# Performance work log

Measured on AMD Instinct MI355X. Metric: run time of the kernel, lower is better.

## Reference

```python
import jax, jax.numpy as jnp
import numpy as np

D_MODEL = 1024
NUM_HEADS = 16
DEPTH = D_MODEL // NUM_HEADS


def setup_inputs() -> dict:
    key = jax.random.key(0)
    ks = jax.random.split(key, 9)
    B, S = 2, 2048
    s = 1.0 / np.sqrt(D_MODEL)
    inp = {
        "inputs": jax.random.normal(ks[0], (B, S, D_MODEL), dtype=jnp.float32),
        "wq": jax.random.normal(ks[1], (D_MODEL, D_MODEL), dtype=jnp.float32) * s,
        "bq": jnp.zeros((D_MODEL,), dtype=jnp.float32),
        "wk": jax.random.normal(ks[2], (D_MODEL, D_MODEL), dtype=jnp.float32) * s,
        "bk": jnp.zeros((D_MODEL,), dtype=jnp.float32),
        "wv": jax.random.normal(ks[3], (D_MODEL, D_MODEL), dtype=jnp.float32) * s,
        "bv": jnp.zeros((D_MODEL,), dtype=jnp.float32),
        "wo": jax.random.normal(ks[4], (D_MODEL, D_MODEL), dtype=jnp.float32) * s,
        "bo": jnp.zeros((D_MODEL,), dtype=jnp.float32),
    }
    return inp


def _split_heads(x, B):
    # [B, S, D] -> [B, H, S, depth]
    S = x.shape[1]
    return x.reshape(B, S, NUM_HEADS, DEPTH).transpose(0, 2, 1, 3)


def reference(inputs, wq, bq, wk, bk, wv, bv, wo, bo):
    B, S, _ = inputs.shape
    q = _split_heads(inputs @ wq + bq, B)  # [B,H,S,d]
    k = _split_heads(inputs @ wk + bk, B)
    v = _split_heads(inputs @ wv + bv, B)
    scale = 1.0 / jnp.sqrt(jnp.asarray(DEPTH, dtype=inputs.dtype))
    logits = jnp.einsum("bhqd,bhkd->bhqk", q, k) * scale  # [B,H,S,S]
    attn = jax.nn.softmax(logits, axis=-1)
    out = jnp.einsum("bhqk,bhkd->bhqd", attn, v)  # [B,H,S,d]
    out = out.transpose(0, 2, 1, 3).reshape(B, S, D_MODEL)
    return out @ wo + bo
```

## Files before the change

kernel.cpp:

```cpp
#include <hip/hip_runtime.h>
#include <math.h>

#define SEQ     2048
#define DM      1024
#define NH      16
#define DEPTH   64
#define MTOT    4096

typedef __attribute__((ext_vector_type(8))) __bf16 bf16x8;
typedef __attribute__((ext_vector_type(4))) float  f32x4;
typedef __attribute__((ext_vector_type(4))) short  short4v;

static __device__ inline short f2bf(float f) {
    union { float f; unsigned u; } v; v.f = f;
    unsigned r = v.u + 0x7FFFu + ((v.u >> 16) & 1u);
    return (short)(r >> 16);
}
static __device__ inline unsigned bfbits(float f) {
    union { float f; unsigned u; } v; v.f = f;
    return (v.u + 0x7FFFu + ((v.u >> 16) & 1u)) >> 16;
}
static __device__ inline unsigned bfbits_fast(float f) {
    union { float f; unsigned u; } v; v.f = f;
    return (v.u + 0x8000u) >> 16;
}

#define GLOBAL_AS(p) ((const __attribute__((address_space(1))) void*)(p))
#define LDS_AS(p)    ((__attribute__((address_space(3))) void*)(p))

#define K2  0.18033688011112043f
#define C2 -17.31234049066756f
#define EXP2(x) __builtin_amdgcn_exp2f(x)

#define DMA_SRC_C8(lane)  ((((lane) & 3) ^ (((lane) >> 3) & 3)) * 8)
#define FRAG_C8(lx,quad)  ((((quad) ^ (((lx) >> 1) & 3))) * 8)

__global__ __launch_bounds__(256)
void prep(const float* __restrict__ X,
          const float* __restrict__ w0, const float* __restrict__ w1,
          const float* __restrict__ w2, const float* __restrict__ w3,
          short* __restrict__ Xb,
          short* __restrict__ o0, short* __restrict__ o1,
          short* __restrict__ o2, short* __restrict__ o3) {
    const int t = threadIdx.x;
    const int z = blockIdx.z;
    if (z >= 4) {
        int r0 = (z - 4) * 1024 + blockIdx.x * 64;
        int c0 = blockIdx.y * 64;
        #pragma unroll
        for (int i = 0; i < 4; i++) {
            int row = r0 + i * 16 + (t >> 4);
            int c4  = c0 + (t & 15) * 4;
            float4 v = *(const float4*)&X[(size_t)row * DM + c4];
            short4v o; o.x = f2bf(v.x); o.y = f2bf(v.y); o.z = f2bf(v.z); o.w = f2bf(v.w);
            *(short4v*)&Xb[(size_t)row * DM + c4] = o;
        }
        return;
    }
    const float* W; short* O;
    switch (z) {
        case 0: W = w0; O = o0; break;
        case 1: W = w1; O = o1; break;
        case 2: W = w2; O = o2; break;
        default: W = w3; O = o3; break;
    }
    __shared__ float Tf[64][65];
    const int k0 = blockIdx.x * 64, n0 = blockIdx.y * 64;
    #pragma unroll
    for (int i = 0; i < 4; i++) {
        int row = i * 16 + (t >> 4);
        int c4  = (t & 15) * 4;
        float4 v = *(const float4*)&W[(size_t)(k0 + row) * DM + n0 + c4];
        Tf[row][c4 + 0] = v.x; Tf[row][c4 + 1] = v.y;
        Tf[row][c4 + 2] = v.z; Tf[row][c4 + 3] = v.w;
    }
    __syncthreads();
    #pragma unroll
    for (int i = 0; i < 4; i++) {
        int nrow = i * 16 + (t >> 4);
        int kc4  = (t & 15) * 4;
        short4v o;
        o.x = f2bf(Tf[kc4 + 0][nrow]); o.y = f2bf(Tf[kc4 + 1][nrow]);
        o.z = f2bf(Tf[kc4 + 2][nrow]); o.w = f2bf(Tf[kc4 + 3][nrow]);
        *(short4v*)&O[(size_t)(n0 + nrow) * DM + k0 + kc4] = o;
    }
}

__global__ __launch_bounds__(256)
void gemm_qkv(const short* __restrict__ Xb,
              const short* __restrict__ Wqt, const short* __restrict__ Wkt,
              const short* __restrict__ Wvt,
              const float* __restrict__ bq, const float* __restrict__ bk,
              const float* __restrict__ bv,
              short* __restrict__ Qw, short* __restrict__ Kw,
              short* __restrict__ Vtw) {
    const int z = blockIdx.z;
    const short* A; const short* B; const float* bias;
    if (z == 0)      { A = Xb;  B = Wqt; bias = bq; }
    else if (z == 1) { A = Xb;  B = Wkt; bias = bk; }
    else             { A = Wvt; B = Xb;  bias = bv; }
    const int bx = blockIdx.x;
    int m0, n0;
    if (z < 2) { n0 = (bx & 7) * 128; m0 = (bx >> 3) * 128; }
    else       { m0 = (bx & 7) * 128; n0 = (bx >> 3) * 128; }

    __shared__ short As[128 * 32];
    __shared__ short Bs[128 * 32];
    const int t = threadIdx.x, lane = t & 63, w = t >> 6;
    const int lx = lane & 15, quad = lane >> 4;
    const int wm = (w & 1) * 64, wn = (w >> 1) * 64;
    const int r = lane >> 2;
    const int cs8 = DMA_SRC_C8(lane);

    f32x4 acc[4][4];
    #pragma unroll
    for (int i = 0; i < 4; i++)
        #pragma unroll
        for (int j = 0; j < 4; j++)
            acc[i][j] = (f32x4){0.f, 0.f, 0.f, 0.f};

    const int fa = FRAG_C8(lx, quad);

    for (int k0 = 0; k0 < DM; k0 += 32) {
        #pragma unroll
        for (int j = 0; j < 2; j++) {
            int rb = (w * 2 + j) * 16;
            __builtin_amdgcn_global_load_lds(
                GLOBAL_AS(A + (size_t)(m0 + rb + r) * DM + k0 + cs8),
                LDS_AS(As + rb * 32), 16, 0, 0);
            __builtin_amdgcn_global_load_lds(
                GLOBAL_AS(B + (size_t)(n0 + rb + r) * DM + k0 + cs8),
                LDS_AS(Bs + rb * 32), 16, 0, 0);
        }
        __syncthreads();

        bf16x8 af[4], bfr[4];
        #pragma unroll
        for (int mt = 0; mt < 4; mt++)
            af[mt] = *(bf16x8*)&As[(wm + mt * 16 + lx) * 32 + fa];
        #pragma unroll
        for (int nt = 0; nt < 4; nt++)
            bfr[nt] = *(bf16x8*)&Bs[(wn + nt * 16 + lx) * 32 + fa];
        #pragma unroll
        for (int mt = 0; mt < 4; mt++)
            #pragma unroll
            for (int nt = 0; nt < 4; nt++)
                acc[mt][nt] = __builtin_amdgcn_mfma_f32_16x16x32_bf16(
                    af[mt], bfr[nt], acc[mt][nt], 0, 0, 0);
        __syncthreads();
    }

    if (z < 2) {
        short* Cp = (z == 0) ? Qw : Kw;
        #pragma unroll
        for (int mt = 0; mt < 4; mt++)
            #pragma unroll
            for (int nt = 0; nt < 4; nt++)
                #pragma unroll
                for (int reg = 0; reg < 4; reg++) {
                    int row = m0 + wm + mt * 16 + quad * 4 + reg;
                    int col = n0 + wn + nt * 16 + lx;
                    Cp[(size_t)row * DM + col] = f2bf(acc[mt][nt][reg] + bias[col]);
                }
    } else {
        int colbase = n0 + wn;
        int bsel    = colbase >> 11;
        int scolb   = colbase & 2047;
        int kb      = scolb & ~63;
        short* Vbh  = Vtw + (size_t)bsel * ((size_t)NH * DEPTH * SEQ);
        #pragma unroll
        for (int mt = 0; mt < 4; mt++) {
            #pragma unroll
            for (int reg = 0; reg < 4; reg++) {
                int row = m0 + wm + mt * 16 + quad * 4 + reg;
                float bb = bias[row];
                unsigned lo = bfbits(acc[mt][0][reg] + bb) | (bfbits(acc[mt][1][reg] + bb) << 16);
                unsigned hi = bfbits(acc[mt][2][reg] + bb) | (bfbits(acc[mt][3][reg] + bb) << 16);
                size_t base = (size_t)row * SEQ + kb + 2 * lx;
                *(unsigned*)&Vbh[base]      = lo;
                *(unsigned*)&Vbh[base + 32] = hi;
            }
        }
    }
}

__global__ __launch_bounds__(256)
void gemm_out(const short* __restrict__ A, const short* __restrict__ B,
              const float* __restrict__ bias, float* __restrict__ C) {
    __shared__ short As[128 * 32];
    __shared__ short Bs[64 * 32];
    const int t = threadIdx.x, lane = t & 63, w = t >> 6;
    const int lx = lane & 15, quad = lane >> 4;
    const int n0 = blockIdx.x * 64, m0 = blockIdx.y * 128;
    const int wm = (w & 1) * 64, wn = (w >> 1) * 32;
    const int r = lane >> 2;
    const int cs8 = DMA_SRC_C8(lane);
    const int fa  = FRAG_C8(lx, quad);

    f32x4 acc[4][2];
    #pragma unroll
    for (int i = 0; i < 4; i++)
        #pragma unroll
        for (int j = 0; j < 2; j++)
            acc[i][j] = (f32x4){0.f, 0.f, 0.f, 0.f};

    for (int k0 = 0; k0 < DM; k0 += 32) {
        #pragma unroll
        for (int j = 0; j < 2; j++) {
            int rb = w * 32 + j * 16;
            __builtin_amdgcn_global_load_lds(
                GLOBAL_AS(A + (size_t)(m0 + rb + r) * DM + k0 + cs8),
                LDS_AS(As + rb * 32), 16, 0, 0);
        }
        {
            int rb = w * 16;
            __builtin_amdgcn_global_load_lds(
                GLOBAL_AS(B + (size_t)(n0 + rb + r) * DM + k0 + cs8),
                LDS_AS(Bs + rb * 32), 16, 0, 0);
        }
        __syncthreads();

        bf16x8 af[4], bfr[2];
        #pragma unroll
        for (int mt = 0; mt < 4; mt++)
            af[mt] = *(bf16x8*)&As[(wm + mt * 16 + lx) * 32 + fa];
        #pragma unroll
        for (int nt = 0; nt < 2; nt++)
            bfr[nt] = *(bf16x8*)&Bs[(wn + nt * 16 + lx) * 32 + fa];
        #pragma unroll
        for (int mt = 0; mt < 4; mt++)
            #pragma unroll
            for (int nt = 0; nt < 2; nt++)
                acc[mt][nt] = __builtin_amdgcn_mfma_f32_16x16x32_bf16(
                    af[mt], bfr[nt], acc[mt][nt], 0, 0, 0);
        __syncthreads();
    }

    #pragma unroll
    for (int mt = 0; mt < 4; mt++)
        #pragma unroll
        for (int nt = 0; nt < 2; nt++)
            #pragma unroll
            for (int reg = 0; reg < 4; reg++) {
                int row = m0 + wm + mt * 16 + quad * 4 + reg;
                int col = n0 + wn + nt * 16 + lx;
                C[(size_t)row * DM + col] = acc[mt][nt][reg] + bias[col];
            }
}

__global__ __launch_bounds__(256)
void flash_mfma(const short* __restrict__ Q, const short* __restrict__ K,
                const short* __restrict__ Vt, short* __restrict__ O) {
    __shared__ short Ks[2][64 * 32];
    __shared__ short Vs[2][64 * 32];
    __shared__ short Ps[128 * 72];

    const int t = threadIdx.x, lane = t & 63, w = t >> 6;
    const int lx = lane & 15, quad = lane >> 4;
    const int h = blockIdx.y, bb = blockIdx.z;
    const int q0 = blockIdx.x * 128;
    const int r = lane >> 2;
    const int cs8 = DMA_SRC_C8(lane);
    const int fa  = FRAG_C8(lx, quad);

    bf16x8 qa[2][2];
    #pragma unroll
    for (int mt = 0; mt < 2; mt++)
        #pragma unroll
        for (int ks = 0; ks < 2; ks++)
            qa[mt][ks] = *(const bf16x8*)&Q[(size_t)(bb * SEQ + q0 + w * 32 + mt * 16 + lx) * DM
                                            + h * DEPTH + ks * 32 + quad * 8];

    f32x4 of[2][4];
    float l_acc[2][4];
    #pragma unroll
    for (int mt = 0; mt < 2; mt++) {
        #pragma unroll
        for (int dt = 0; dt < 4; dt++) of[mt][dt] = (f32x4){0.f, 0.f, 0.f, 0.f};
        #pragma unroll
        for (int reg = 0; reg < 4; reg++) l_acc[mt][reg] = 0.f;
    }

    const short* Kb = K  + (size_t)bb * SEQ * DM + h * DEPTH;
    const short* Vb = Vt + (size_t)(bb * NH + h) * DEPTH * SEQ;

    for (int kt = 0; kt < SEQ / 64; kt++) {
        __syncthreads();
        const int kbase = kt * 64;
        {
            const short* kg = Kb + (size_t)(kbase + w * 16 + r) * DM;
            __builtin_amdgcn_global_load_lds(GLOBAL_AS(kg + cs8),      LDS_AS(&Ks[0][w * 16 * 32]), 16, 0, 0);
            __builtin_amdgcn_global_load_lds(GLOBAL_AS(kg + 32 + cs8), LDS_AS(&Ks[1][w * 16 * 32]), 16, 0, 0);
            const short* vg = Vb + (size_t)(w * 16 + r) * SEQ + kbase;
            __builtin_amdgcn_global_load_lds(GLOBAL_AS(vg + cs8),      LDS_AS(&Vs[0][w * 16 * 32]), 16, 0, 0);
            __builtin_amdgcn_global_load_lds(GLOBAL_AS(vg + 32 + cs8), LDS_AS(&Vs[1][w * 16 * 32]), 16, 0, 0);
        }
        __syncthreads();

        f32x4 s[2][4];
        #pragma unroll
        for (int mt = 0; mt < 2; mt++)
            #pragma unroll
            for (int nt = 0; nt < 4; nt++)
                s[mt][nt] = (f32x4){0.f, 0.f, 0.f, 0.f};
        #pragma unroll
        for (int ks = 0; ks < 2; ks++) {
            bf16x8 kb[4];
            #pragma unroll
            for (int nt = 0; nt < 4; nt++)
                kb[nt] = *(bf16x8*)&Ks[ks][(nt * 16 + lx) * 32 + fa];
            #pragma unroll
            for (int mt = 0; mt < 2; mt++)
                #pragma unroll
                for (int nt = 0; nt < 4; nt++)
                    s[mt][nt] = __builtin_amdgcn_mfma_f32_16x16x32_bf16(
                        qa[mt][ks], kb[nt], s[mt][nt], 0, 0, 0);
        }

        #pragma unroll
        for (int mt = 0; mt < 2; mt++) {
            #pragma unroll
            for (int reg = 0; reg < 4; reg++) {
                float p0 = EXP2(fmaf(s[mt][0][reg], K2, C2));
                float p1 = EXP2(fmaf(s[mt][1][reg], K2, C2));
                float p2 = EXP2(fmaf(s[mt][2][reg], K2, C2));
                float p3 = EXP2(fmaf(s[mt][3][reg], K2, C2));
                l_acc[mt][reg] += (p0 + p1) + (p2 + p3);
                int rowoff = (w * 32 + mt * 16 + quad * 4 + reg) * 72;
                unsigned pk01 = bfbits_fast(p0) | (bfbits_fast(p1) << 16);
                unsigned pk23 = bfbits_fast(p2) | (bfbits_fast(p3) << 16);
                *(unsigned*)&Ps[rowoff + 2 * lx]      = pk01;
                *(unsigned*)&Ps[rowoff + 32 + 2 * lx] = pk23;
            }
        }

        #pragma unroll
        for (int ks = 0; ks < 2; ks++) {
            bf16x8 vb[4], pa[2];
            #pragma unroll
            for (int dt = 0; dt < 4; dt++)
                vb[dt] = *(bf16x8*)&Vs[ks][(dt * 16 + lx) * 32 + fa];
            #pragma unroll
            for (int mt = 0; mt < 2; mt++)
                pa[mt] = *(bf16x8*)&Ps[(w * 32 + mt * 16 + lx) * 72 + ks * 32 + quad * 8];
            #pragma unroll
            for (int mt = 0; mt < 2; mt++)
                #pragma unroll
                for (int dt = 0; dt < 4; dt++)
                    of[mt][dt] = __builtin_amdgcn_mfma_f32_16x16x32_bf16(
                        pa[mt], vb[dt], of[mt][dt], 0, 0, 0);
        }
    }

    #pragma unroll
    for (int mt = 0; mt < 2; mt++) {
        #pragma unroll
        for (int reg = 0; reg < 4; reg++) {
            float l = l_acc[mt][reg];
            l += __shfl_xor(l, 1);
            l += __shfl_xor(l, 2);
            l += __shfl_xor(l, 4);
            l += __shfl_xor(l, 8);
            float inv = 1.0f / l;
            size_t row = (size_t)bb * SEQ + q0 + w * 32 + mt * 16 + quad * 4 + reg;
            #pragma unroll
            for (int dt = 0; dt < 4; dt++)
                O[row * DM + h * DEPTH + dt * 16 + lx] = f2bf(of[mt][dt][reg] * inv);
        }
    }
}

extern "C" void kernel_launch(void* const* d_in, const int* in_sizes, int n_in,
                              void* d_out, int out_size, void* d_ws, size_t ws_size,
                              hipStream_t stream) {
    const float* X  = (const float*)d_in[0];
    const float* wq = (const float*)d_in[1];
    const float* bq = (const float*)d_in[2];
    const float* wk = (const float*)d_in[3];
    const float* bk = (const float*)d_in[4];
    const float* wv = (const float*)d_in[5];
    const float* bv = (const float*)d_in[6];
    const float* wo = (const float*)d_in[7];
    const float* bo = (const float*)d_in[8];
    float* out = (float*)d_out;

    short* Xb  = (short*)d_ws;
    short* Wqt = Xb  + (size_t)MTOT * DM;
    short* Wkt = Wqt + (size_t)DM * DM;
    short* Wvt = Wkt + (size_t)DM * DM;
    short* Wot = Wvt + (size_t)DM * DM;
    short* Qw  = Wot + (size_t)DM * DM;
    short* Kw  = Qw  + (size_t)MTOT * DM;
    short* Vtw = Kw  + (size_t)MTOT * DM;
    short* AO  = Vtw + (size_t)MTOT * DM;

    hipLaunchKernelGGL(prep, dim3(16, 16, 8), dim3(256), 0, stream,
                       X, wq, wk, wv, wo, Xb, Wqt, Wkt, Wvt, Wot);

    hipLaunchKernelGGL(gemm_qkv, dim3(256, 1, 3), dim3(256), 0, stream,
                       Xb, Wqt, Wkt, Wvt, bq, bk, bv, Qw, Kw, Vtw);

    hipLaunchKernelGGL(flash_mfma, dim3(SEQ / 128, NH, 2), dim3(256), 0, stream,
                       Qw, Kw, Vtw, AO);

    hipLaunchKernelGGL(gemm_out, dim3(16, 32), dim3(256), 0, stream,
                       AO, Wot, bo, out);
}
```

Before: 211.3 us.

## Double K-depth per stage in GEMMs and widen attention key tile to 128

The projection and output GEMMs now stage 64-wide K slices per barrier pair, with a new 8-way XOR swizzle, halving the number of sync rounds. The flash attention kernel processes 128 keys per iteration instead of 64, halving barriers and load rounds but raising register and LDS use. The Q/K GEMM epilogue also hoists bias loads and packs two bf16 values per 32-bit store. The larger tiles may reduce occupancy.

```diff
diff --git a/kernel.cpp b/kernel.cpp
--- a/kernel.cpp
+++ b/kernel.cpp
@@ -34,6 +34,8 @@
 
 #define DMA_SRC_C8(lane)  ((((lane) & 3) ^ (((lane) >> 3) & 3)) * 8)
 #define FRAG_C8(lx,quad)  ((((quad) ^ (((lx) >> 1) & 3))) * 8)
+#define DMA_SRC64(lane)   ((((lane) & 7) ^ (((lane) >> 3) & 7)) * 8)
+#define FRAG64(lx,c)      ((((c) ^ ((lx) & 7))) * 8)
 
 __global__ __launch_bounds__(256)
 void prep(const float* __restrict__ X,
@@ -104,13 +106,13 @@
     if (z < 2) { n0 = (bx & 7) * 128; m0 = (bx >> 3) * 128; }
     else       { m0 = (bx & 7) * 128; n0 = (bx >> 3) * 128; }
 
-    __shared__ short As[128 * 32];
-    __shared__ short Bs[128 * 32];
+    __shared__ short As[128 * 64];
+    __shared__ short Bs[128 * 64];
     const int t = threadIdx.x, lane = t & 63, w = t >> 6;
     const int lx = lane & 15, quad = lane >> 4;
     const int wm = (w & 1) * 64, wn = (w >> 1) * 64;
-    const int r = lane >> 2;
-    const int cs8 = DMA_SRC_C8(lane);
+    const int r8 = lane >> 3;
+    const int cs = DMA_SRC64(lane);
 
     f32x4 acc[4][4];
     #pragma unroll
@@ -119,54 +121,60 @@
         for (int j = 0; j < 4; j++)
             acc[i][j] = (f32x4){0.f, 0.f, 0.f, 0.f};
 
-    const int fa = FRAG_C8(lx, quad);
-
-    for (int k0 = 0; k0 < DM; k0 += 32) {
-        #pragma unroll
-        for (int j = 0; j < 2; j++) {
-            int rb = (w * 2 + j) * 16;
+    for (int k0 = 0; k0 < DM; k0 += 64) {
+        #pragma unroll
+        for (int j = 0; j < 4; j++) {
+            int rb = w * 32 + j * 8;
             __builtin_amdgcn_global_load_lds(
-                GLOBAL_AS(A + (size_t)(m0 + rb + r) * DM + k0 + cs8),
-                LDS_AS(As + rb * 32), 16, 0, 0);
+                GLOBAL_AS(A + (size_t)(m0 + rb + r8) * DM + k0 + cs),
+                LDS_AS(As + rb * 64), 16, 0, 0);
             __builtin_amdgcn_global_load_lds(
-                GLOBAL_AS(B + (size_t)(n0 + rb + r) * DM + k0 + cs8),
-                LDS_AS(Bs + rb * 32), 16, 0, 0);
-        }
-        __syncthreads();
-
-        bf16x8 af[4], bfr[4];
-        #pragma unroll
-        for (int mt = 0; mt < 4; mt++)
-            af[mt] = *(bf16x8*)&As[(wm + mt * 16 + lx) * 32 + fa];
-        #pragma unroll
-        for (int nt = 0; nt < 4; nt++)
-            bfr[nt] = *(bf16x8*)&Bs[(wn + nt * 16 + lx) * 32 + fa];
-        #pragma unroll
-        for (int mt = 0; mt < 4; mt++)
+                GLOBAL_AS(B + (size_t)(n0 + rb + r8) * DM + k0 + cs),
+                LDS_AS(Bs + rb * 64), 16, 0, 0);
+        }
+        __syncthreads();
+
+        #pragma unroll
+        for (int ks = 0; ks < 2; ks++) {
+            const int fo = FRAG64(lx, ks * 4 + quad);
+            bf16x8 af[4], bfr[4];
+            #pragma unroll
+            for (int mt = 0; mt < 4; mt++)
+                af[mt] = *(bf16x8*)&As[(wm + mt * 16 + lx) * 64 + fo];
             #pragma unroll
             for (int nt = 0; nt < 4; nt++)
-                acc[mt][nt] = __builtin_amdgcn_mfma_f32_16x16x32_bf16(
-                    af[mt], bfr[nt], acc[mt][nt], 0, 0, 0);
+                bfr[nt] = *(bf16x8*)&Bs[(wn + nt * 16 + lx) * 64 + fo];
+            #pragma unroll
+            for (int mt = 0; mt < 4; mt++)
+                #pragma unroll
+                for (int nt = 0; nt < 4; nt++)
+                    acc[mt][nt] = __builtin_amdgcn_mfma_f32_16x16x32_bf16(
+                        af[mt], bfr[nt], acc[mt][nt], 0, 0, 0);
+        }
         __syncthreads();
     }
 
     if (z < 2) {
         short* Cp = (z == 0) ? Qw : Kw;
-        #pragma unroll
-        for (int mt = 0; mt < 4; mt++)
-            #pragma unroll
-            for (int nt = 0; nt < 4; nt++)
-                #pragma unroll
-                for (int reg = 0; reg < 4; reg++) {
-                    int row = m0 + wm + mt * 16 + quad * 4 + reg;
-                    int col = n0 + wn + nt * 16 + lx;
-                    Cp[(size_t)row * DM + col] = f2bf(acc[mt][nt][reg] + bias[col]);
-                }
+        float bi[4];
+        #pragma unroll
+        for (int nt = 0; nt < 4; nt++) bi[nt] = bias[n0 + wn + nt * 16 + lx];
+        #pragma unroll
+        for (int mt = 0; mt < 4; mt++) {
+            #pragma unroll
+            for (int reg = 0; reg < 4; reg++) {
+                int row = m0 + wm + mt * 16 + quad * 4 + reg;
+                unsigned lo = bfbits(acc[mt][0][reg] + bi[0]) | (bfbits(acc[mt][1][reg] + bi[1]) << 16);
+                unsigned hi = bfbits(acc[mt][2][reg] + bi[2]) | (bfbits(acc[mt][3][reg] + bi[3]) << 16);
+                size_t base = (size_t)row * DM + n0 + wn + 2 * lx;
+                *(unsigned*)&Cp[base]      = lo;
+                *(unsigned*)&Cp[base + 32] = hi;
+            }
+        }
     } else {
         int colbase = n0 + wn;
         int bsel    = colbase >> 11;
-        int scolb   = colbase & 2047;
-        int kb      = scolb & ~63;
+        int kb      = (colbase & 2047) & ~63;
         short* Vbh  = Vtw + (size_t)bsel * ((size_t)NH * DEPTH * SEQ);
         #pragma unroll
         for (int mt = 0; mt < 4; mt++) {
@@ -187,15 +195,14 @@
 __global__ __launch_bounds__(256)
 void gemm_out(const short* __restrict__ A, const short* __restrict__ B,
               const float* __restrict__ bias, float* __restrict__ C) {
-    __shared__ short As[128 * 32];
-    __shared__ short Bs[64 * 32];
+    __shared__ short As[128 * 64];
+    __shared__ short Bs[64 * 64];
     const int t = threadIdx.x, lane = t & 63, w = t >> 6;
     const int lx = lane & 15, quad = lane >> 4;
     const int n0 = blockIdx.x * 64, m0 = blockIdx.y * 128;
     const int wm = (w & 1) * 64, wn = (w >> 1) * 32;
-    const int r = lane >> 2;
-    const int cs8 = DMA_SRC_C8(lane);
-    const int fa  = FRAG_C8(lx, quad);
+    const int r8 = lane >> 3;
+    const int cs = DMA_SRC64(lane);
 
     f32x4 acc[4][2];
     #pragma unroll
@@ -204,35 +211,40 @@
         for (int j = 0; j < 2; j++)
             acc[i][j] = (f32x4){0.f, 0.f, 0.f, 0.f};
 
-    for (int k0 = 0; k0 < DM; k0 += 32) {
+    for (int k0 = 0; k0 < DM; k0 += 64) {
+        #pragma unroll
+        for (int j = 0; j < 4; j++) {
+            int rb = w * 32 + j * 8;
+            __builtin_amdgcn_global_load_lds(
+                GLOBAL_AS(A + (size_t)(m0 + rb + r8) * DM + k0 + cs),
+                LDS_AS(As + rb * 64), 16, 0, 0);
+        }
         #pragma unroll
         for (int j = 0; j < 2; j++) {
-            int rb = w * 32 + j * 16;
+            int rb = w * 16 + j * 8;
             __builtin_amdgcn_global_load_lds(
-                GLOBAL_AS(A + (size_t)(m0 + rb + r) * DM + k0 + cs8),
-                LDS_AS(As + rb * 32), 16, 0, 0);
-        }
-        {
-            int rb = w * 16;
-            __builtin_amdgcn_global_load_lds(
-                GLOBAL_AS(B + (size_t)(n0 + rb + r) * DM + k0 + cs8),
-                LDS_AS(Bs + rb * 32), 16, 0, 0);
-        }
-        __syncthreads();
-
-        bf16x8 af[4], bfr[2];
-        #pragma unroll
-        for (int mt = 0; mt < 4; mt++)
-            af[mt] = *(bf16x8*)&As[(wm + mt * 16 + lx) * 32 + fa];
-        #pragma unroll
-        for (int nt = 0; nt < 2; nt++)
-            bfr[nt] = *(bf16x8*)&Bs[(wn + nt * 16 + lx) * 32 + fa];
-        #pragma unroll
-        for (int mt = 0; mt < 4; mt++)
+                GLOBAL_AS(B + (size_t)(n0 + rb + r8) * DM + k0 + cs),
+                LDS_AS(Bs + rb * 64), 16, 0, 0);
+        }
+        __syncthreads();
+
+        #pragma unroll
+        for (int ks = 0; ks < 2; ks++) {
+            const int fo = FRAG64(lx, ks * 4 + quad);
+            bf16x8 af[4], bfr[2];
+            #pragma unroll
+            for (int mt = 0; mt < 4; mt++)
+                af[mt] = *(bf16x8*)&As[(wm + mt * 16 + lx) * 64 + fo];
             #pragma unroll
             for (int nt = 0; nt < 2; nt++)
-                acc[mt][nt] = __builtin_amdgcn_mfma_f32_16x16x32_bf16(
-                    af[mt], bfr[nt], acc[mt][nt], 0, 0, 0);
+                bfr[nt] = *(bf16x8*)&Bs[(wn + nt * 16 + lx) * 64 + fo];
+            #pragma unroll
+            for (int mt = 0; mt < 4; mt++)
+                #pragma unroll
+                for (int nt = 0; nt < 2; nt++)
+                    acc[mt][nt] = __builtin_amdgcn_mfma_f32_16x16x32_bf16(
+                        af[mt], bfr[nt], acc[mt][nt], 0, 0, 0);
+        }
         __syncthreads();
     }
 
@@ -251,16 +263,16 @@
 __global__ __launch_bounds__(256)
 void flash_mfma(const short* __restrict__ Q, const short* __restrict__ K,
                 const short* __restrict__ Vt, short* __restrict__ O) {
-    __shared__ short Ks[2][64 * 32];
-    __shared__ short Vs[2][64 * 32];
-    __shared__ short Ps[128 * 72];
+    __shared__ short Ks[2][128 * 32];
+    __shared__ short Vs[4][64 * 32];
+    __shared__ short Ps[128 * 136];
 
     const int t = threadIdx.x, lane = t & 63, w = t >> 6;
     const int lx = lane & 15, quad = lane >> 4;
     const int h = blockIdx.y, bb = blockIdx.z;
     const int q0 = blockIdx.x * 128;
-    const int r = lane >> 2;
-    const int cs8 = DMA_SRC_C8(lane);
+    const int r4 = lane >> 2;
+    const int cs  = DMA_SRC_C8(lane);
     const int fa  = FRAG_C8(lx, quad);
 
     bf16x8 qa[2][2];
@@ -284,35 +296,44 @@
     const short* Kb = K  + (size_t)bb * SEQ * DM + h * DEPTH;
     const short* Vb = Vt + (size_t)(bb * NH + h) * DEPTH * SEQ;
 
-    for (int kt = 0; kt < SEQ / 64; kt++) {
-        __syncthreads();
-        const int kbase = kt * 64;
-        {
-            const short* kg = Kb + (size_t)(kbase + w * 16 + r) * DM;
-            __builtin_amdgcn_global_load_lds(GLOBAL_AS(kg + cs8),      LDS_AS(&Ks[0][w * 16 * 32]), 16, 0, 0);
-            __builtin_amdgcn_global_load_lds(GLOBAL_AS(kg + 32 + cs8), LDS_AS(&Ks[1][w * 16 * 32]), 16, 0, 0);
-            const short* vg = Vb + (size_t)(w * 16 + r) * SEQ + kbase;
-            __builtin_amdgcn_global_load_lds(GLOBAL_AS(vg + cs8),      LDS_AS(&Vs[0][w * 16 * 32]), 16, 0, 0);
-            __builtin_amdgcn_global_load_lds(GLOBAL_AS(vg + 32 + cs8), LDS_AS(&Vs[1][w * 16 * 32]), 16, 0, 0);
-        }
-        __syncthreads();
-
-        f32x4 s[2][4];
+    for (int kt = 0; kt < SEQ / 128; kt++) {
+        __syncthreads();
+        const int kbase = kt * 128;
+        #pragma unroll
+        for (int ks = 0; ks < 2; ks++) {
+            #pragma unroll
+            for (int j = 0; j < 2; j++) {
+                int rb = w * 32 + j * 16;
+                __builtin_amdgcn_global_load_lds(
+                    GLOBAL_AS(Kb + (size_t)(kbase + rb + r4) * DM + ks * 32 + cs),
+                    LDS_AS(&Ks[ks][rb * 32]), 16, 0, 0);
+            }
+        }
+        #pragma unroll
+        for (int c = 0; c < 4; c++) {
+            int rb = w * 16;
+            __builtin_amdgcn_global_load_lds(
+                GLOBAL_AS(Vb + (size_t)(rb + r4) * SEQ + kbase + c * 32 + cs),
+                LDS_AS(&Vs[c][rb * 32]), 16, 0, 0);
+        }
+        __syncthreads();
+
+        f32x4 s[2][8];
         #pragma unroll
         for (int mt = 0; mt < 2; mt++)
             #pragma unroll
-            for (int nt = 0; nt < 4; nt++)
+            for (int nt = 0; nt < 8; nt++)
                 s[mt][nt] = (f32x4){0.f, 0.f, 0.f, 0.f};
         #pragma unroll
         for (int ks = 0; ks < 2; ks++) {
-            bf16x8 kb[4];
-            #pragma unroll
-            for (int nt = 0; nt < 4; nt++)
+            bf16x8 kb[8];
+            #pragma unroll
+            for (int nt = 0; nt < 8; nt++)
                 kb[nt] = *(bf16x8*)&Ks[ks][(nt * 16 + lx) * 32 + fa];
             #pragma unroll
             for (int mt = 0; mt < 2; mt++)
                 #pragma unroll
-                for (int nt = 0; nt < 4; nt++)
+                for (int nt = 0; nt < 8; nt++)
                     s[mt][nt] = __builtin_amdgcn_mfma_f32_16x16x32_bf16(
                         qa[mt][ks], kb[nt], s[mt][nt], 0, 0, 0);
         }
@@ -321,28 +342,32 @@
         for (int mt = 0; mt < 2; mt++) {
             #pragma unroll
             for (int reg = 0; reg < 4; reg++) {
-                float p0 = EXP2(fmaf(s[mt][0][reg], K2, C2));
-                float p1 = EXP2(fmaf(s[mt][1][reg], K2, C2));
-                float p2 = EXP2(fmaf(s[mt][2][reg], K2, C2));
-                float p3 = EXP2(fmaf(s[mt][3][reg], K2, C2));
-                l_acc[mt][reg] += (p0 + p1) + (p2 + p3);
-                int rowoff = (w * 32 + mt * 16 + quad * 4 + reg) * 72;
-                unsigned pk01 = bfbits_fast(p0) | (bfbits_fast(p1) << 16);
-                unsigned pk23 = bfbits_fast(p2) | (bfbits_fast(p3) << 16);
-                *(unsigned*)&Ps[rowoff + 2 * lx]      = pk01;
-                *(unsigned*)&Ps[rowoff + 32 + 2 * lx] = pk23;
+                float p[8];
+                float lsum = 0.f;
+                #pragma unroll
+                for (int nt = 0; nt < 8; nt++) {
+                    p[nt] = EXP2(fmaf(s[mt][nt][reg], K2, C2));
+                    lsum += p[nt];
+                }
+                l_acc[mt][reg] += lsum;
+                int rowoff = (w * 32 + mt * 16 + quad * 4 + reg) * 136 + 2 * lx;
+                #pragma unroll
+                for (int pr = 0; pr < 4; pr++) {
+                    unsigned pk = bfbits_fast(p[2 * pr]) | (bfbits_fast(p[2 * pr + 1]) << 16);
+                    *(unsigned*)&Ps[rowoff + pr * 32] = pk;
+                }
             }
         }
 
         #pragma unroll
-        for (int ks = 0; ks < 2; ks++) {
+        for (int c = 0; c < 4; c++) {
             bf16x8 vb[4], pa[2];
             #pragma unroll
             for (int dt = 0; dt < 4; dt++)
-                vb[dt] = *(bf16x8*)&Vs[ks][(dt * 16 + lx) * 32 + fa];
+                vb[dt] = *(bf16x8*)&Vs[c][(dt * 16 + lx) * 32 + fa];
             #pragma unroll
             for (int mt = 0; mt < 2; mt++)
-                pa[mt] = *(bf16x8*)&Ps[(w * 32 + mt * 16 + lx) * 72 + ks * 32 + quad * 8];
+                pa[mt] = *(bf16x8*)&Ps[(w * 32 + mt * 16 + lx) * 136 + c * 32 + quad * 8];
             #pragma unroll
             for (int mt = 0; mt < 2; mt++)
                 #pragma unroll
```

New measurement: 208.1 us. About the same (-1.5%).
